# Optimization experiments

Hardware: AMD Instinct MI355X
Metric: run time of the kernel (lower is better)

Reference implementation:

```python
import jax, jax.numpy as jnp
import numpy as np


def ternary_quantize(w):
    # threshold = 0.7 * mean(|w|); maps w to {-1, 0, +1}
    threshold = 0.7 * jnp.sum(jnp.abs(w)) / w.size
    return jnp.sign(jnp.sign(w + threshold) + jnp.sign(w - threshold))


def setup_inputs() -> dict:
    key = jax.random.key(0)
    k1, k2, k3 = jax.random.split(key, 3)
    B, N = 4096, 8192
    x = jax.random.normal(k1, (B, N), dtype=jnp.float32)
    kernel = jax.random.normal(k2, (N,), dtype=jnp.float32)
    bias = jax.random.normal(k3, (N,), dtype=jnp.float32)
    return {"x": x, "kernel": kernel, "bias": bias}


def reference(x, kernel, bias):
    # Original: y = x @ diag(ternary(kernel)) + bias.
    # Matmul by a diagonal matrix is exactly a per-column scale; we compute
    # the identical math as a fused elementwise scale + bias add.
    q = ternary_quantize(kernel)          # [N] in {-1, 0, 1}
    return x * q[None, :] + bias[None, :]  # [B, N]
```

## Files before the change

### kernel.cpp

```cpp
#include <hip/hip_runtime.h>

typedef float f32x4 __attribute__((ext_vector_type(4)));

__device__ __forceinline__ void nt_store(f32x4 v, f32x4* p) {
    __builtin_nontemporal_store(v, p);
}

__device__ __forceinline__ float tern(float w, float t) {
    return (fabsf(w) >= t) ? copysignf(1.f, w) : 0.f;
}

__global__ __launch_bounds__(1024) void threshold_kernel(
    const float* __restrict__ w, float* __restrict__ t_out, int n) {
    const int tid = threadIdx.x;
    const f32x4* w4 = reinterpret_cast<const f32x4*>(w);
    const int n4 = n >> 2;
    float s = 0.f;
    for (int i = tid; i < n4; i += 1024) {
        const f32x4 v = w4[i];
        s += fabsf(v.x) + fabsf(v.y) + fabsf(v.z) + fabsf(v.w);
    }
    #pragma unroll
    for (int off = 32; off > 0; off >>= 1) s += __shfl_xor(s, off, 64);
    __shared__ float partial[16];
    if ((tid & 63) == 0) partial[tid >> 6] = s;
    __syncthreads();
    if (tid == 0) {
        float tot = 0.f;
        #pragma unroll
        for (int k = 0; k < 16; ++k) tot += partial[k];
        t_out[0] = 0.7f * tot / (float)n;
    }
}

__global__ __launch_bounds__(256) void scale_bias_stream4(
    const f32x4* __restrict__ x, const float* __restrict__ w,
    const f32x4* __restrict__ bias4, f32x4* __restrict__ out,
    const float* __restrict__ t_ptr, int n, long total4) {
    const int tid = threadIdx.x;
    const float t = t_ptr[0];

    const int n4 = n >> 2;
    const long i0 = (long)blockIdx.x * blockDim.x + tid;
    const long stride = (long)gridDim.x * blockDim.x;
    const int c = (int)(i0 & (long)(n4 - 1));

    const f32x4 wv = reinterpret_cast<const f32x4*>(w)[c];
    f32x4 qv;
    qv.x = tern(wv.x, t);
    qv.y = tern(wv.y, t);
    qv.z = tern(wv.z, t);
    qv.w = tern(wv.w, t);
    const f32x4 bv = bias4[c];

    for (long i = i0; i < total4; i += 4 * stride) {
        const f32x4 a = x[i];
        const f32x4 b = x[i + stride];
        const f32x4 c2 = x[i + 2 * stride];
        const f32x4 d = x[i + 3 * stride];
        nt_store(a * qv + bv, &out[i]);
        nt_store(b * qv + bv, &out[i + stride]);
        nt_store(c2 * qv + bv, &out[i + 2 * stride]);
        nt_store(d * qv + bv, &out[i + 3 * stride]);
    }
}

__global__ __launch_bounds__(256) void scale_bias_stream(
    const f32x4* __restrict__ x, const float* __restrict__ w,
    const f32x4* __restrict__ bias4, f32x4* __restrict__ out,
    const float* __restrict__ t_ptr, int n, long total4) {
    const int tid = threadIdx.x;
    const float t = t_ptr[0];
    const int n4 = n >> 2;
    const long i0 = (long)blockIdx.x * blockDim.x + tid;
    const long stride = (long)gridDim.x * blockDim.x;
    const int c = (int)(i0 & (long)(n4 - 1));
    const f32x4 wv = reinterpret_cast<const f32x4*>(w)[c];
    f32x4 qv;
    qv.x = tern(wv.x, t);
    qv.y = tern(wv.y, t);
    qv.z = tern(wv.z, t);
    qv.w = tern(wv.w, t);
    const f32x4 bv = bias4[c];
    for (long i = i0; i < total4; i += stride) {
        nt_store(x[i] * qv + bv, &out[i]);
    }
}

extern "C" void kernel_launch(void* const* d_in, const int* in_sizes, int n_in,
                              void* d_out, int out_size, void* d_ws, size_t ws_size,
                              hipStream_t stream) {
    const float* x      = (const float*)d_in[0];
    const float* kernel = (const float*)d_in[1];
    const float* bias   = (const float*)d_in[2];
    float* out = (float*)d_out;
    float* t_ws = (float*)d_ws;

    const int N = in_sizes[1];
    const long total4 = (long)out_size / 4;
    const long stride = 2048L * 256;

    threshold_kernel<<<1, 1024, 0, stream>>>(kernel, t_ws, N);

    if ((N & (N - 1)) == 0 && total4 % (4 * stride) == 0) {
        scale_bias_stream4<<<2048, 256, 0, stream>>>(
            (const f32x4*)x, kernel, (const f32x4*)bias, (f32x4*)out,
            t_ws, N, total4);
    } else {
        scale_bias_stream<<<2048, 256, 0, stream>>>(
            (const f32x4*)x, kernel, (const f32x4*)bias, (f32x4*)out,
            t_ws, N, total4);
    }
}
```

Baseline: 53.38 us.

## Fuse threshold reduction into streaming kernel, recomputed per block

Drops the separate single-block threshold kernel. Each of the 2048 blocks of the streaming kernel now recomputes the full 8192-element abs-sum reduction itself, which removes one launch and the serialized dependency between kernels. In exchange every block re-reads the 32 KB weight vector and adds a syncthreads, and the 4-way unrolled main loop becomes single-step. The fallback path is also made general for non-power-of-two N by recomputing the column index and quantized weights per iteration.

```diff
diff --git a/kernel.cpp b/kernel.cpp
--- a/kernel.cpp
+++ b/kernel.cpp
@@ -10,16 +10,50 @@
     return (fabsf(w) >= t) ? copysignf(1.f, w) : 0.f;
 }
 
+__global__ __launch_bounds__(256) void fused_cheap(
+    const f32x4* __restrict__ x, const float* __restrict__ w,
+    const f32x4* __restrict__ bias4, f32x4* __restrict__ out,
+    int n, long total4) {
+    const int tid = threadIdx.x;
+    const f32x4* w4 = reinterpret_cast<const f32x4*>(w);
+
+    float s = 0.f;
+    #pragma unroll
+    for (int k = 0; k < 8; ++k) {
+        const f32x4 v = w4[tid + k * 256];
+        s += fabsf(v.x) + fabsf(v.y) + fabsf(v.z) + fabsf(v.w);
+    }
+    #pragma unroll
+    for (int off = 32; off > 0; off >>= 1) s += __shfl_xor(s, off, 64);
+    __shared__ float partial[4];
+    if ((tid & 63) == 0) partial[tid >> 6] = s;
+    __syncthreads();
+    const float t = 0.7f * (partial[0] + partial[1] + partial[2] + partial[3])
+                    / (float)n;
+
+    const int n4 = n >> 2;
+    const long i0 = (long)blockIdx.x * blockDim.x + tid;
+    const long stride = (long)gridDim.x * blockDim.x;
+    const int c = (int)(i0 & (long)(n4 - 1));
+
+    const f32x4 wv = w4[c];
+    f32x4 qv;
+    qv.x = tern(wv.x, t);
+    qv.y = tern(wv.y, t);
+    qv.z = tern(wv.z, t);
+    qv.w = tern(wv.w, t);
+    const f32x4 bv = bias4[c];
+
+    for (long i = i0; i < total4; i += stride) {
+        nt_store(x[i] * qv + bv, &out[i]);
+    }
+}
+
 __global__ __launch_bounds__(1024) void threshold_kernel(
     const float* __restrict__ w, float* __restrict__ t_out, int n) {
     const int tid = threadIdx.x;
-    const f32x4* w4 = reinterpret_cast<const f32x4*>(w);
-    const int n4 = n >> 2;
     float s = 0.f;
-    for (int i = tid; i < n4; i += 1024) {
-        const f32x4 v = w4[i];
-        s += fabsf(v.x) + fabsf(v.y) + fabsf(v.z) + fabsf(v.w);
-    }
+    for (int i = tid; i < n; i += 1024) s += fabsf(w[i]);
     #pragma unroll
     for (int off = 32; off > 0; off >>= 1) s += __shfl_xor(s, off, 64);
     __shared__ float partial[16];
@@ -33,38 +67,6 @@
     }
 }
 
-__global__ __launch_bounds__(256) void scale_bias_stream4(
-    const f32x4* __restrict__ x, const float* __restrict__ w,
-    const f32x4* __restrict__ bias4, f32x4* __restrict__ out,
-    const float* __restrict__ t_ptr, int n, long total4) {
-    const int tid = threadIdx.x;
-    const float t = t_ptr[0];
-
-    const int n4 = n >> 2;
-    const long i0 = (long)blockIdx.x * blockDim.x + tid;
-    const long stride = (long)gridDim.x * blockDim.x;
-    const int c = (int)(i0 & (long)(n4 - 1));
-
-    const f32x4 wv = reinterpret_cast<const f32x4*>(w)[c];
-    f32x4 qv;
-    qv.x = tern(wv.x, t);
-    qv.y = tern(wv.y, t);
-    qv.z = tern(wv.z, t);
-    qv.w = tern(wv.w, t);
-    const f32x4 bv = bias4[c];
-
-    for (long i = i0; i < total4; i += 4 * stride) {
-        const f32x4 a = x[i];
-        const f32x4 b = x[i + stride];
-        const f32x4 c2 = x[i + 2 * stride];
-        const f32x4 d = x[i + 3 * stride];
-        nt_store(a * qv + bv, &out[i]);
-        nt_store(b * qv + bv, &out[i + stride]);
-        nt_store(c2 * qv + bv, &out[i + 2 * stride]);
-        nt_store(d * qv + bv, &out[i + 3 * stride]);
-    }
-}
-
 __global__ __launch_bounds__(256) void scale_bias_stream(
     const f32x4* __restrict__ x, const float* __restrict__ w,
     const f32x4* __restrict__ bias4, f32x4* __restrict__ out,
@@ -74,16 +76,15 @@
     const int n4 = n >> 2;
     const long i0 = (long)blockIdx.x * blockDim.x + tid;
     const long stride = (long)gridDim.x * blockDim.x;
-    const int c = (int)(i0 & (long)(n4 - 1));
-    const f32x4 wv = reinterpret_cast<const f32x4*>(w)[c];
-    f32x4 qv;
-    qv.x = tern(wv.x, t);
-    qv.y = tern(wv.y, t);
-    qv.z = tern(wv.z, t);
-    qv.w = tern(wv.w, t);
-    const f32x4 bv = bias4[c];
     for (long i = i0; i < total4; i += stride) {
-        nt_store(x[i] * qv + bv, &out[i]);
+        const int c = (int)(i % n4);
+        const f32x4 wv = reinterpret_cast<const f32x4*>(w)[c];
+        f32x4 qv;
+        qv.x = tern(wv.x, t);
+        qv.y = tern(wv.y, t);
+        qv.z = tern(wv.z, t);
+        qv.w = tern(wv.w, t);
+        nt_store(x[i] * qv + bias4[c], &out[i]);
     }
 }
 
@@ -100,13 +101,12 @@
     const long total4 = (long)out_size / 4;
     const long stride = 2048L * 256;
 
-    threshold_kernel<<<1, 1024, 0, stream>>>(kernel, t_ws, N);
-
-    if ((N & (N - 1)) == 0 && total4 % (4 * stride) == 0) {
-        scale_bias_stream4<<<2048, 256, 0, stream>>>(
+    if (N == 8192 && stride % (N / 4) == 0) {
+        fused_cheap<<<2048, 256, 0, stream>>>(
             (const f32x4*)x, kernel, (const f32x4*)bias, (f32x4*)out,
-            t_ws, N, total4);
+            N, total4);
     } else {
+        threshold_kernel<<<1, 1024, 0, stream>>>(kernel, t_ws, N);
         scale_bias_stream<<<2048, 256, 0, stream>>>(
             (const f32x4*)x, kernel, (const f32x4*)bias, (f32x4*)out,
             t_ws, N, total4);
```

Result: faster. 47.40 us (-11.2%).
